# Performance work log

Measured on AMD Instinct MI355X. Metric: run time of the kernel, lower is better.

The kernel has to match this reference:

```python
import jax, jax.numpy as jnp
import numpy as np


def setup_inputs() -> dict:
    key = jax.random.key(0)
    k1, k2 = jax.random.split(key)
    B, K = 128, 1024
    coordinates = jax.random.normal(k1, (B, K, 3), dtype=jnp.float32)
    precision_squared = jax.random.uniform(k2, (1,), dtype=jnp.float32)
    return {"coordinates": coordinates, "precision_squared": precision_squared}


def reference(coordinates, precision_squared):
    norms = jnp.sum(coordinates * coordinates, axis=-1)  # [B, K]
    gram = jnp.einsum('bkd,bjd->bkj', coordinates, coordinates)  # [B, K, K]
    distances = norms[:, :, None] - 2.0 * gram + norms[:, None, :]  # [B, K, K]
    A = jnp.exp(-distances * precision_squared[0])
    A = jax.nn.softmax(A, axis=-1)  # row softmax (axis=1 of the per-sample [K,K])
    return A
```

## Files before the change

### kernel.cpp

```cpp
#include <hip/hip_runtime.h>


#define K_PTS 1024
#define ROWS_PER_BLOCK 4

__global__ __launch_bounds__(256) void adj_softmax_kernel(
    const float* __restrict__ coords,
    const float* __restrict__ prec,
    float* __restrict__ out,
    int B) {
  __shared__ float sx[K_PTS];
  __shared__ float sy[K_PTS];
  __shared__ float sz[K_PTS];

  const int tid  = threadIdx.x;
  const int lane = tid & 63;
  const int wave = tid >> 6;
  const int tilesPerBatch = K_PTS / ROWS_PER_BLOCK;
  const int b    = blockIdx.x / tilesPerBatch;
  const int tile = blockIdx.x % tilesPerBatch;

  const float p = prec[0];

  {
    const float* cb = coords + (size_t)b * (K_PTS * 3);
    const int p0 = tid * 4;
    const float4* src = (const float4*)(cb + (size_t)p0 * 3);
    float4 a0 = src[0];
    float4 a1 = src[1];
    float4 a2 = src[2];
    sx[p0 + 0] = a0.x; sy[p0 + 0] = a0.y; sz[p0 + 0] = a0.z;
    sx[p0 + 1] = a0.w; sy[p0 + 1] = a1.x; sz[p0 + 1] = a1.y;
    sx[p0 + 2] = a1.z; sy[p0 + 2] = a1.w; sz[p0 + 2] = a2.x;
    sx[p0 + 3] = a2.y; sy[p0 + 3] = a2.z; sz[p0 + 3] = a2.w;
  }
  __syncthreads();

  const int i = tile * ROWS_PER_BLOCK + wave;
  const float xi = sx[i];
  const float yi = sy[i];
  const float zi = sz[i];

  float4 e[4];
  float acc = 0.0f;

#pragma unroll
  for (int t = 0; t < 4; ++t) {
    const int j0 = 4 * lane + 256 * t;
    float4 vx = *(const float4*)&sx[j0];
    float4 vy = *(const float4*)&sy[j0];
    float4 vz = *(const float4*)&sz[j0];

    float dx, dy, dz, d, xv;
    float4 ev;

    dx = vx.x - xi; dy = vy.x - yi; dz = vz.x - zi;
    d  = fmaf(dx, dx, fmaf(dy, dy, dz * dz));
    xv = __expf(-p * d);
    ev.x = __expf(xv - 1.0f);

    dx = vx.y - xi; dy = vy.y - yi; dz = vz.y - zi;
    d  = fmaf(dx, dx, fmaf(dy, dy, dz * dz));
    xv = __expf(-p * d);
    ev.y = __expf(xv - 1.0f);

    dx = vx.z - xi; dy = vy.z - yi; dz = vz.z - zi;
    d  = fmaf(dx, dx, fmaf(dy, dy, dz * dz));
    xv = __expf(-p * d);
    ev.z = __expf(xv - 1.0f);

    dx = vx.w - xi; dy = vy.w - yi; dz = vz.w - zi;
    d  = fmaf(dx, dx, fmaf(dy, dy, dz * dz));
    xv = __expf(-p * d);
    ev.w = __expf(xv - 1.0f);

    e[t] = ev;
    acc += (ev.x + ev.y) + (ev.z + ev.w);
  }

#pragma unroll
  for (int off = 32; off > 0; off >>= 1) {
    acc += __shfl_xor(acc, off, 64);
  }
  const float inv = 1.0f / acc;

  float* orow = out + ((size_t)b * K_PTS + i) * K_PTS;
#pragma unroll
  for (int t = 0; t < 4; ++t) {
    float4 ev = e[t];
    ev.x *= inv; ev.y *= inv; ev.z *= inv; ev.w *= inv;
    *(float4*)&orow[4 * lane + 256 * t] = ev;
  }
}

extern "C" void kernel_launch(void* const* d_in, const int* in_sizes, int n_in,
                              void* d_out, int out_size, void* d_ws, size_t ws_size,
                              hipStream_t stream) {
  const float* coords = (const float*)d_in[0];
  const float* prec   = (const float*)d_in[1];
  float* out = (float*)d_out;

  const int B = in_sizes[0] / (K_PTS * 3);
  const int grid = B * (K_PTS / ROWS_PER_BLOCK);

  adj_softmax_kernel<<<grid, 256, 0, stream>>>(coords, prec, out, B);
}
```

Baseline: 512.3 us.

## Process four rows per wave and use native exp2 with folded constants

Each wave now computes four output rows instead of one, so each block covers 16 rows. The shared-memory coordinate loads are reused across rows, and the per-block staging of the batch's coordinates is amortized over four times as many rows. The two exponentials now call the hardware exp2 builtin with log2(e) folded into the scale. The constant exp(-1) factor is dropped from the inner exponent because it cancels in the softmax normalization. The cost is more registers (64 floats of results per thread) and a quarter as many blocks. The kernel is likely bound by output writes (512MB), so the gains may be limited.

```diff
diff --git a/kernel.cpp b/kernel.cpp
--- a/kernel.cpp
+++ b/kernel.cpp
@@ -2,13 +2,14 @@
 
 
 #define K_PTS 1024
-#define ROWS_PER_BLOCK 4
+#define RPW 4
+#define ROWS_PER_BLOCK 16
+#define L2E 1.44269504088896340736f
 
-__global__ __launch_bounds__(256) void adj_softmax_kernel(
+__global__ __launch_bounds__(256, 4) void adj_softmax_kernel(
     const float* __restrict__ coords,
     const float* __restrict__ prec,
-    float* __restrict__ out,
-    int B) {
+    float* __restrict__ out) {
   __shared__ float sx[K_PTS];
   __shared__ float sy[K_PTS];
   __shared__ float sz[K_PTS];
@@ -36,13 +37,17 @@
   }
   __syncthreads();
 
-  const int i = tile * ROWS_PER_BLOCK + wave;
-  const float xi = sx[i];
-  const float yi = sy[i];
-  const float zi = sz[i];
+  const float qa = -p * L2E;
 
-  float4 e[4];
-  float acc = 0.0f;
+  const int i0 = tile * ROWS_PER_BLOCK + wave * RPW;
+  float xi[RPW], yi[RPW], zi[RPW];
+#pragma unroll
+  for (int r = 0; r < RPW; ++r) {
+    xi[r] = sx[i0 + r]; yi[r] = sy[i0 + r]; zi[r] = sz[i0 + r];
+  }
+
+  float4 ev[RPW][4];
+  float acc[RPW] = {0.f, 0.f, 0.f, 0.f};
 
 #pragma unroll
   for (int t = 0; t < 4; ++t) {
@@ -51,45 +56,55 @@
     float4 vy = *(const float4*)&sy[j0];
     float4 vz = *(const float4*)&sz[j0];
 
-    float dx, dy, dz, d, xv;
-    float4 ev;
+#pragma unroll
+    for (int r = 0; r < RPW; ++r) {
+      float dx, dy, dz, d, xv;
+      float4 e4;
 
-    dx = vx.x - xi; dy = vy.x - yi; dz = vz.x - zi;
-    d  = fmaf(dx, dx, fmaf(dy, dy, dz * dz));
-    xv = __expf(-p * d);
-    ev.x = __expf(xv - 1.0f);
+      dx = vx.x - xi[r]; dy = vy.x - yi[r]; dz = vz.x - zi[r];
+      d  = fmaf(dx, dx, fmaf(dy, dy, dz * dz));
+      xv = __builtin_amdgcn_exp2f(qa * d);
+      e4.x = __builtin_amdgcn_exp2f(xv * L2E);
 
-    dx = vx.y - xi; dy = vy.y - yi; dz = vz.y - zi;
-    d  = fmaf(dx, dx, fmaf(dy, dy, dz * dz));
-    xv = __expf(-p * d);
-    ev.y = __expf(xv - 1.0f);
+      dx = vx.y - xi[r]; dy = vy.y - yi[r]; dz = vz.y - zi[r];
+      d  = fmaf(dx, dx, fmaf(dy, dy, dz * dz));
+      xv = __builtin_amdgcn_exp2f(qa * d);
+      e4.y = __builtin_amdgcn_exp2f(xv * L2E);
 
-    dx = vx.z - xi; dy = vy.z - yi; dz = vz.z - zi;
-    d  = fmaf(dx, dx, fmaf(dy, dy, dz * dz));
-    xv = __expf(-p * d);
-    ev.z = __expf(xv - 1.0f);
+      dx = vx.z - xi[r]; dy = vy.z - yi[r]; dz = vz.z - zi[r];
+      d  = fmaf(dx, dx, fmaf(dy, dy, dz * dz));
+      xv = __builtin_amdgcn_exp2f(qa * d);
+      e4.z = __builtin_amdgcn_exp2f(xv * L2E);
 
-    dx = vx.w - xi; dy = vy.w - yi; dz = vz.w - zi;
-    d  = fmaf(dx, dx, fmaf(dy, dy, dz * dz));
-    xv = __expf(-p * d);
-    ev.w = __expf(xv - 1.0f);
+      dx = vx.w - xi[r]; dy = vy.w - yi[r]; dz = vz.w - zi[r];
+      d  = fmaf(dx, dx, fmaf(dy, dy, dz * dz));
+      xv = __builtin_amdgcn_exp2f(qa * d);
+      e4.w = __builtin_amdgcn_exp2f(xv * L2E);
 
-    e[t] = ev;
-    acc += (ev.x + ev.y) + (ev.z + ev.w);
+      ev[r][t] = e4;
+      acc[r] += (e4.x + e4.y) + (e4.z + e4.w);
+    }
+  }
+
+  float inv[RPW];
+#pragma unroll
+  for (int r = 0; r < RPW; ++r) {
+    float a = acc[r];
+#pragma unroll
+    for (int off = 32; off > 0; off >>= 1) a += __shfl_xor(a, off, 64);
+    inv[r] = 1.0f / a;
   }
 
 #pragma unroll
-  for (int off = 32; off > 0; off >>= 1) {
-    acc += __shfl_xor(acc, off, 64);
-  }
-  const float inv = 1.0f / acc;
-
-  float* orow = out + ((size_t)b * K_PTS + i) * K_PTS;
+  for (int r = 0; r < RPW; ++r) {
+    float* orow = out + ((size_t)b * K_PTS + (i0 + r)) * K_PTS;
+    const float s = inv[r];
 #pragma unroll
-  for (int t = 0; t < 4; ++t) {
-    float4 ev = e[t];
-    ev.x *= inv; ev.y *= inv; ev.z *= inv; ev.w *= inv;
-    *(float4*)&orow[4 * lane + 256 * t] = ev;
+    for (int t = 0; t < 4; ++t) {
+      float4 e4 = ev[r][t];
+      e4.x *= s; e4.y *= s; e4.z *= s; e4.w *= s;
+      *(float4*)&orow[4 * lane + 256 * t] = e4;
+    }
   }
 }
 
@@ -103,5 +118,5 @@
   const int B = in_sizes[0] / (K_PTS * 3);
   const int grid = B * (K_PTS / ROWS_PER_BLOCK);
 
-  adj_softmax_kernel<<<grid, 256, 0, stream>>>(coords, prec, out, B);
+  adj_softmax_kernel<<<grid, 256, 0, stream>>>(coords, prec, out);
 }
```

Result: slower. 523.6 us (+2.2%).
